# Kernel tuning notes

Hardware: AMD Instinct MI355X
Metric: run time of the kernel (lower is better)

## Reference

```python
import jax, jax.numpy as jnp
import numpy as np

H, W = 480, 640
ICP_W = 10.0
N_ITER = 20
FTOL = 1e-3
XTOL = 1e-8
DIST_THR = 200.0 / 15.0
NORMAL_THR = 0.94


def _skew(w):
    z = jnp.zeros((), w.dtype)
    return jnp.stack([
        jnp.stack([z, -w[2], w[1]]),
        jnp.stack([w[2], z, -w[0]]),
        jnp.stack([-w[1], w[0], z]),
    ])


def _exp_se3(xi):
    # xi = (v, w); SE3 exponential map (lie_se3_to_SE3)
    v, w = xi[:3], xi[3:]
    th2 = jnp.sum(w * w)
    th = jnp.sqrt(th2)
    small = th < 1e-8
    ths = jnp.where(small, 1.0, th)
    A = jnp.where(small, 1.0 - th2 / 6.0, jnp.sin(ths) / ths)
    B = jnp.where(small, 0.5 - th2 / 24.0, (1.0 - jnp.cos(ths)) / (ths * ths))
    C = jnp.where(small, 1.0 / 6.0 - th2 / 120.0, (ths - jnp.sin(ths)) / (ths * ths * ths))
    Wx = _skew(w)
    W2 = Wx @ Wx
    R = jnp.eye(3, dtype=xi.dtype) + A * Wx + B * W2
    V = jnp.eye(3, dtype=xi.dtype) + B * Wx + C * W2
    t = V @ v
    T = jnp.eye(4, dtype=xi.dtype)
    T = T.at[:3, :3].set(R).at[:3, 3].set(t)
    return T


def _bilinear(img, u, v):
    # img [H,W]; u,v [N] float pixel coords
    u0 = jnp.floor(u)
    v0 = jnp.floor(v)
    du = u - u0
    dv = v - v0
    u0i = jnp.clip(u0.astype(jnp.int32), 0, W - 1)
    u1i = jnp.clip(u0i + 1, 0, W - 1)
    v0i = jnp.clip(v0.astype(jnp.int32), 0, H - 1)
    v1i = jnp.clip(v0i + 1, 0, H - 1)
    I00 = img[v0i, u0i]; I01 = img[v0i, u1i]
    I10 = img[v1i, u0i]; I11 = img[v1i, u1i]
    return (I00 * (1 - du) + I01 * du) * (1 - dv) + (I10 * (1 - du) + I11 * du) * dv


def _forward(depth_ref, normals_ref, gray_ref, gray_target, points_target, normals_target, intrinsics):
    dt = depth_ref.dtype
    fx, fy = intrinsics[0, 0], intrinsics[1, 1]
    cx, cy = intrinsics[0, 2], intrinsics[1, 2]
    vv, uu = jnp.meshgrid(jnp.arange(H, dtype=dt), jnp.arange(W, dtype=dt), indexing='ij')
    Z = depth_ref
    # ref PointCloud.from_depth: backprojection [N,3]
    P = jnp.stack([(uu - cx) / fx * Z, (vv - cy) / fy * Z, Z], -1).reshape(-1, 3)
    Nr = normals_ref.reshape(-1, 3)
    Ir = gray_ref.reshape(-1)
    gy_img, gx_img = jnp.gradient(gray_target)  # d/dv, d/du
    Nflt = jnp.asarray(H * W, dt)

    def step(carry, _):
        x, conv, cost = carry
        T = _exp_se3(x)
        R, t = T[:3, :3], T[:3, 3]
        Pt = P @ R.T + t  # transformed ref points [N,3]
        Zt = Pt[:, 2]
        okz = Zt > 1e-6
        Zs = jnp.where(okz, Zt, 1.0)
        u = fx * Pt[:, 0] / Zs + cx
        v = fy * Pt[:, 1] / Zs + cy
        inb = okz & (u >= 0) & (u <= W - 1) & (v >= 0) & (v <= H - 1)
        ui = jnp.clip(jnp.round(u).astype(jnp.int32), 0, W - 1)
        vi = jnp.clip(jnp.round(v).astype(jnp.int32), 0, H - 1)
        # --- ICP point-to-plane, projective association ---
        q = points_target[vi, ui]    # [N,3]
        nq = normals_target[vi, ui]  # [N,3]
        d = Pt - q
        nref_rot = Nr @ R.T
        valid_icp = inb & (jnp.sum(d * d, -1) < DIST_THR ** 2) & (jnp.sum(nref_rot * nq, -1) > NORMAL_THR)
        m_icp = valid_icp.astype(dt)
        r_icp = jnp.sum(nq * d, -1) * m_icp                              # [N]
        J_icp = jnp.concatenate([nq, jnp.cross(Pt, nq)], -1) * m_icp[:, None]  # [N,6]
        # --- RGB photometric ---
        m_rgb = inb.astype(dt)
        It = _bilinear(gray_target, u, v)
        r_rgb = (It - Ir) * m_rgb
        gxs = _bilinear(gx_img, u, v)
        gys = _bilinear(gy_img, u, v)
        # grad_I * d(projection)/d(point)
        gp = jnp.stack([
            gxs * fx / Zs,
            gys * fy / Zs,
            -(gxs * fx * Pt[:, 0] + gys * fy * Pt[:, 1]) / (Zs * Zs),
        ], -1)
        J_rgb = jnp.concatenate([gp, jnp.cross(Pt, gp)], -1) * m_rgb[:, None]
        # --- normal equations ---
        A = ICP_W * (J_icp.T @ J_icp) + J_rgb.T @ J_rgb
        b = ICP_W * (J_icp.T @ r_icp) + J_rgb.T @ r_rgb
        x0 = jnp.linalg.solve(A + 1e-9 * jnp.eye(6, dtype=dt), b)
        new_cost = ICP_W * jnp.sum(r_icp ** 2) / Nflt + jnp.sum(r_rgb ** 2) / Nflt
        c = conv | (new_cost < FTOL) | (jnp.linalg.norm(x0) < XTOL * (XTOL + jnp.linalg.norm(x)))
        x_new = jnp.where(c, x, x - x0)
        cost_new = jnp.where(conv, cost, new_cost)
        return (x_new, c, cost_new), None

    init = (jnp.zeros(6, dt), jnp.array(False), jnp.asarray(0.0, dt))
    (x, conv, cost), _ = jax.lax.scan(step, init, None, length=N_ITER)
    return _exp_se3(x), cost


def setup_inputs() -> dict:
    key = jax.random.key(0)
    ks = jax.random.split(key, 6)
    intrinsics = jnp.array([[525.0, 0.0, 319.5], [0.0, 525.0, 239.5], [0.0, 0.0, 1.0]], jnp.float32)
    fx, fy, cx, cy = 525.0, 525.0, 319.5, 239.5
    depth_ref = 0.5 + 1.5 * jax.random.uniform(ks[0], (H, W), jnp.float32)
    depth_t = 0.5 + 1.5 * jax.random.uniform(ks[1], (H, W), jnp.float32)
    vv, uu = jnp.meshgrid(jnp.arange(H, dtype=jnp.float32), jnp.arange(W, dtype=jnp.float32), indexing='ij')
    points_target = jnp.stack([(uu - cx) / fx * depth_t, (vv - cy) / fy * depth_t, depth_t], -1)
    def mk_normals(k):
        n = 0.1 * jax.random.normal(k, (H, W, 3), jnp.float32) + jnp.array([0.0, 0.0, -1.0])
        return n / jnp.linalg.norm(n, axis=-1, keepdims=True)
    normals_ref = mk_normals(ks[2])
    normals_target = mk_normals(ks[3])
    gray_ref = jax.random.uniform(ks[4], (H, W), jnp.float32)
    gray_target = jax.random.uniform(ks[5], (H, W), jnp.float32)
    return {
        'depth_ref': depth_ref,
        'normals_ref': normals_ref,
        'gray_ref': gray_ref,
        'gray_target': gray_target,
        'points_target': points_target,
        'normals_target': normals_target,
        'intrinsics': intrinsics,
    }


def reference(depth_ref, normals_ref, gray_ref, gray_target, points_target, normals_target, intrinsics):
    return _forward(depth_ref, normals_ref, gray_ref, gray_target, points_target, normals_target, intrinsics)
```

## Files before the change

### kernel.cpp

```cpp
#include <hip/hip_runtime.h>
#include <math.h>

#define HH 480
#define WW 640
#define NPIX (HH*WW)
#define NACC 29
#define TPB_B 512
#define NB_B 600
#define TPB_C 256
#define PB 600
#define CH 75

#define WS_P 512
#define WS_G4 18432
#define WS_NR (WS_G4 + NPIX*4)
#define WS_PZ (WS_NR + NPIX*4)
#define WS_BIG_END (WS_PZ + NPIX*4)

__device__ __forceinline__ float gradu(const float* g, int v, int u) {
    const float* row = g + v * WW;
    if (u == 0)      return row[1] - row[0];
    if (u == WW - 1) return row[WW - 1] - row[WW - 2];
    return 0.5f * (row[u + 1] - row[u - 1]);
}
__device__ __forceinline__ float gradv(const float* g, int v, int u) {
    if (v == 0)      return g[WW + u] - g[u];
    if (v == HH - 1) return g[(HH - 1) * WW + u] - g[(HH - 2) * WW + u];
    return 0.5f * (g[(v + 1) * WW + u] - g[(v - 1) * WW + u]);
}

__device__ void exp_se3_f32(const float* xi, float* T) {
    float v0 = xi[0], v1 = xi[1], v2 = xi[2];
    float w0 = xi[3], w1 = xi[4], w2 = xi[5];
    float th2 = w0 * w0 + w1 * w1 + w2 * w2;
    float th = sqrtf(th2);
    bool small = th < 1e-8f;
    float ths = small ? 1.0f : th;
    float A = small ? (1.0f - th2 / 6.0f) : (sinf(ths) / ths);
    float B = small ? (0.5f - th2 / 24.0f) : ((1.0f - cosf(ths)) / (ths * ths));
    float C = small ? (1.0f / 6.0f - th2 / 120.0f) : ((ths - sinf(ths)) / (ths * ths * ths));
    float Wx[9] = { 0.f, -w2,  w1,
                    w2,  0.f, -w0,
                   -w1,  w0,  0.f };
    float W2[9];
    #pragma unroll
    for (int i = 0; i < 3; i++)
        #pragma unroll
        for (int j = 0; j < 3; j++) {
            float s = 0.f;
            #pragma unroll
            for (int k = 0; k < 3; k++) s += Wx[i * 3 + k] * Wx[k * 3 + j];
            W2[i * 3 + j] = s;
        }
    float R[9], V[9];
    #pragma unroll
    for (int i = 0; i < 9; i++) {
        float id = (i == 0 || i == 4 || i == 8) ? 1.0f : 0.0f;
        R[i] = id + A * Wx[i] + B * W2[i];
        V[i] = id + B * Wx[i] + C * W2[i];
    }
    float t0 = V[0] * v0 + V[1] * v1 + V[2] * v2;
    float t1 = V[3] * v0 + V[4] * v1 + V[5] * v2;
    float t2 = V[6] * v0 + V[7] * v1 + V[8] * v2;
    T[0] = R[0]; T[1] = R[1]; T[2]  = R[2]; T[3]  = t0;
    T[4] = R[3]; T[5] = R[4]; T[6]  = R[5]; T[7]  = t1;
    T[8] = R[6]; T[9] = R[7]; T[10] = R[8]; T[11] = t2;
    T[12] = 0.f; T[13] = 0.f; T[14] = 0.f; T[15] = 1.f;
}

__device__ __forceinline__ void accum_point(float* acc, const float* J, float r, float w, int costslot) {
    int k = 0;
    #pragma unroll
    for (int i = 0; i < 6; i++) {
        #pragma unroll
        for (int j = i; j < 6; j++) { acc[k] += w * (J[i] * J[j]); k++; }
        acc[21 + i] += w * (J[i] * r);
    }
    acc[costslot] += r * r;
}

template <int PACKED>
__global__ __launch_bounds__(TPB_B) void pack_init(
    const float* __restrict__ depth_ref,
    const float* __restrict__ normals_ref,
    const float* __restrict__ gray_target,
    const float* __restrict__ points_target,
    const float* __restrict__ normals_target,
    float* __restrict__ ws)
{
    if (blockIdx.x == 0 && threadIdx.x == 0) {
        ws[0] = 1.f; ws[1] = 0.f; ws[2] = 0.f;
        ws[3] = 0.f; ws[4] = 1.f; ws[5] = 0.f;
        ws[6] = 0.f; ws[7] = 0.f; ws[8] = 1.f;
        ws[9] = 0.f; ws[10] = 0.f; ws[11] = 0.f;
        ws[12] = 0.f; ws[13] = 0.f;
        #pragma unroll
        for (int i = 0; i < 6; i++) ws[16 + i] = 0.f;
    }
    if (PACKED) {
        int p = blockIdx.x * TPB_B + threadIdx.x;
        int v = p / WW, u = p - v * WW;
        float4* g4  = (float4*)(ws + WS_G4);
        float4* nr4 = (float4*)(ws + WS_NR);
        float4* pz4 = (float4*)(ws + WS_PZ);
        float4 c;
        c.x = gray_target[p];
        c.y = gradu(gray_target, v, u);
        c.z = gradv(gray_target, v, u);
        c.w = 0.f;
        g4[p] = c;
        float4 n;
        n.x = normals_ref[3 * p];
        n.y = normals_ref[3 * p + 1];
        n.z = normals_ref[3 * p + 2];
        n.w = depth_ref[p];
        nr4[p] = n;
        float4 z;
        z.x = points_target[3 * p + 2];
        z.y = normals_target[3 * p];
        z.z = normals_target[3 * p + 1];
        z.w = normals_target[3 * p + 2];
        pz4[p] = z;
    }
}

template <int PACKED>
__global__ __launch_bounds__(TPB_B) void map_reduce(
    const float* __restrict__ depth_ref,
    const float* __restrict__ normals_ref,
    const float* __restrict__ gray_ref,
    const float* __restrict__ gray_target,
    const float* __restrict__ points_target,
    const float* __restrict__ normals_target,
    const float* __restrict__ K,
    float* __restrict__ ws)
{
    const int tid = threadIdx.x;
    const int bid = blockIdx.x;
    const float fx = K[0], cx = K[2], fy = K[4], cy = K[5];
    const float4* g4  = (const float4*)(ws + WS_G4);
    const float4* nr4 = (const float4*)(ws + WS_NR);
    const float4* pz4 = (const float4*)(ws + WS_PZ);

    __shared__ float spose[12];
    __shared__ float lds[8][NACC];
    if (tid < 12) spose[tid] = ws[tid];
    __syncthreads();
    const float R00 = spose[0], R01 = spose[1], R02 = spose[2];
    const float R10 = spose[3], R11 = spose[4], R12 = spose[5];
    const float R20 = spose[6], R21 = spose[7], R22 = spose[8];
    const float t0 = spose[9], t1 = spose[10], t2 = spose[11];

    float acc[NACC];
    #pragma unroll
    for (int i = 0; i < NACC; i++) acc[i] = 0.f;

    {
        int p = bid * TPB_B + tid;
        int vv = p / WW;
        int uu = p - vv * WW;

        float nr0, nr1, nr2, Z;
        if (PACKED) {
            float4 n = nr4[p];
            nr0 = n.x; nr1 = n.y; nr2 = n.z; Z = n.w;
        } else {
            Z = depth_ref[p];
            nr0 = normals_ref[3 * p]; nr1 = normals_ref[3 * p + 1]; nr2 = normals_ref[3 * p + 2];
        }
        float Px = ((float)uu - cx) / fx * Z;
        float Py = ((float)vv - cy) / fy * Z;
        float Pz = Z;
        float Ptx = R00 * Px + R01 * Py + R02 * Pz + t0;
        float Pty = R10 * Px + R11 * Py + R12 * Pz + t1;
        float Ptz = R20 * Px + R21 * Py + R22 * Pz + t2;
        bool okz = Ptz > 1e-6f;
        float Zs = okz ? Ptz : 1.0f;
        float u = fx * Ptx / Zs + cx;
        float v = fy * Pty / Zs + cy;
        bool inb = okz && (u >= 0.f) && (u <= (float)(WW - 1)) && (v >= 0.f) && (v <= (float)(HH - 1));
        if (inb) {
            int ui = (int)rintf(u); ui = ui < 0 ? 0 : (ui > WW - 1 ? WW - 1 : ui);
            int vi = (int)rintf(v); vi = vi < 0 ? 0 : (vi > HH - 1 ? HH - 1 : vi);
            int ti = vi * WW + ui;
            float qx, qy, qz, nqx, nqy, nqz;
            if (PACKED) {
                float4 z = pz4[ti];
                qz = z.x; nqx = z.y; nqy = z.z; nqz = z.w;
                qx = (((float)ui) - cx) / fx * qz;
                qy = (((float)vi) - cy) / fy * qz;
            } else {
                qx = points_target[3 * ti]; qy = points_target[3 * ti + 1]; qz = points_target[3 * ti + 2];
                nqx = normals_target[3 * ti]; nqy = normals_target[3 * ti + 1]; nqz = normals_target[3 * ti + 2];
            }
            float dx = Ptx - qx, dy = Pty - qy, dz = Ptz - qz;
            float nrx = R00 * nr0 + R01 * nr1 + R02 * nr2;
            float nry = R10 * nr0 + R11 * nr1 + R12 * nr2;
            float nrz = R20 * nr0 + R21 * nr1 + R22 * nr2;
            const float DIST2 = (float)((200.0 / 15.0) * (200.0 / 15.0));
            if ((dx * dx + dy * dy + dz * dz) < DIST2 &&
                (nrx * nqx + nry * nqy + nrz * nqz) > 0.94f) {
                float r = nqx * dx + nqy * dy + nqz * dz;
                float J[6] = { nqx, nqy, nqz,
                               Pty * nqz - Ptz * nqy,
                               Ptz * nqx - Ptx * nqz,
                               Ptx * nqy - Pty * nqx };
                accum_point(acc, J, r, 10.0f, 27);
            }
            float u0f = floorf(u), v0f = floorf(v);
            float du = u - u0f, dv = v - v0f;
            int u0 = (int)u0f; u0 = u0 < 0 ? 0 : (u0 > WW - 1 ? WW - 1 : u0);
            int u1 = (u0 + 1 > WW - 1) ? WW - 1 : u0 + 1;
            int v0 = (int)v0f; v0 = v0 < 0 ? 0 : (v0 > HH - 1 ? HH - 1 : v0);
            int v1 = (v0 + 1 > HH - 1) ? HH - 1 : v0 + 1;
            int i00 = v0 * WW + u0, i01 = v0 * WW + u1, i10 = v1 * WW + u0, i11 = v1 * WW + u1;
            float I00, I01, I10, I11, gx00, gx01, gx10, gx11, gy00, gy01, gy10, gy11;
            if (PACKED) {
                float4 c00 = g4[i00], c01 = g4[i01], c10 = g4[i10], c11 = g4[i11];
                I00 = c00.x; gx00 = c00.y; gy00 = c00.z;
                I01 = c01.x; gx01 = c01.y; gy01 = c01.z;
                I10 = c10.x; gx10 = c10.y; gy10 = c10.z;
                I11 = c11.x; gx11 = c11.y; gy11 = c11.z;
            } else {
                const float* g = gray_target;
                I00 = g[i00]; I01 = g[i01]; I10 = g[i10]; I11 = g[i11];
                gx00 = gradu(g, v0, u0); gx01 = gradu(g, v0, u1);
                gx10 = gradu(g, v1, u0); gx11 = gradu(g, v1, u1);
                gy00 = gradv(g, v0, u0); gy01 = gradv(g, v0, u1);
                gy10 = gradv(g, v1, u0); gy11 = gradv(g, v1, u1);
            }
            float It  = (I00 * (1.f - du) + I01 * du) * (1.f - dv) + (I10 * (1.f - du) + I11 * du) * dv;
            float gxs = (gx00 * (1.f - du) + gx01 * du) * (1.f - dv) + (gx10 * (1.f - du) + gx11 * du) * dv;
            float gys = (gy00 * (1.f - du) + gy01 * du) * (1.f - dv) + (gy10 * (1.f - du) + gy11 * du) * dv;
            float rr = It - gray_ref[p];
            float gpx = gxs * fx / Zs;
            float gpy = gys * fy / Zs;
            float gpz = -(gxs * fx * Ptx + gys * fy * Pty) / (Zs * Zs);
            float J[6] = { gpx, gpy, gpz,
                           Pty * gpz - Ptz * gpy,
                           Ptz * gpx - Ptx * gpz,
                           Ptx * gpy - Pty * gpx };
            accum_point(acc, J, rr, 1.0f, 28);
        }
    }

    #pragma unroll
    for (int q = 0; q < NACC; q++) {
        float vq = acc[q];
        #pragma unroll
        for (int off = 32; off >= 1; off >>= 1) vq += __shfl_xor(vq, off);
        acc[q] = vq;
    }
    int wave = tid >> 6;
    int lane = tid & 63;
    if (lane == 0) {
        #pragma unroll
        for (int q = 0; q < NACC; q++) lds[wave][q] = acc[q];
    }
    __syncthreads();
    if (tid < NACC) {
        int q = tid;
        float s = ((lds[0][q] + lds[1][q]) + (lds[2][q] + lds[3][q]))
                + ((lds[4][q] + lds[5][q]) + (lds[6][q] + lds[7][q]));
        ws[WS_P + q * PB + bid] = s;
    }
}

__global__ __launch_bounds__(TPB_C) void solve_update(float* __restrict__ ws,
                                                      float* __restrict__ out,
                                                      int final_iter)
{
    __shared__ double part8[NACC * 8];
    __shared__ double sums[NACC];
    int tid = threadIdx.x;
    const float* part = ws + WS_P;
    if (tid < NACC * 8) {
        int q = tid >> 3, s = tid & 7;
        const float* row = part + q * PB + s * CH;
        double a0 = 0.0, a1 = 0.0, a2 = 0.0, a3 = 0.0;
        int i = 0;
        for (; i + 4 <= CH; i += 4) {
            a0 += (double)row[i];
            a1 += (double)row[i + 1];
            a2 += (double)row[i + 2];
            a3 += (double)row[i + 3];
        }
        for (; i < CH; i++) a0 += (double)row[i];
        part8[tid] = ((a0 + a1) + (a2 + a3));
    }
    __syncthreads();
    if (tid < NACC) {
        double sm = 0.0;
        #pragma unroll
        for (int s = 0; s < 8; s++) sm += part8[tid * 8 + s];
        sums[tid] = sm;
    }
    __syncthreads();
    if (tid == 0) {
        double M[6][7];
        int k = 0;
        for (int i = 0; i < 6; i++)
            for (int j = i; j < 6; j++) { M[i][j] = sums[k]; M[j][i] = sums[k]; k++; }
        for (int i = 0; i < 6; i++) { M[i][6] = sums[21 + i]; M[i][i] += 1e-9; }
        double new_cost = 10.0 * sums[27] / (double)NPIX + sums[28] / (double)NPIX;

        for (int c = 0; c < 6; c++) {
            int piv = c; double mx = fabs(M[c][c]);
            for (int r2 = c + 1; r2 < 6; r2++) {
                double a = fabs(M[r2][c]);
                if (a > mx) { mx = a; piv = r2; }
            }
            if (piv != c)
                for (int j2 = 0; j2 < 7; j2++) { double tmp = M[c][j2]; M[c][j2] = M[piv][j2]; M[piv][j2] = tmp; }
            double inv = 1.0 / M[c][c];
            for (int r2 = c + 1; r2 < 6; r2++) {
                double f = M[r2][c] * inv;
                for (int j2 = c; j2 < 7; j2++) M[r2][j2] -= f * M[c][j2];
            }
        }
        double x0[6];
        for (int i = 5; i >= 0; i--) {
            double s = M[i][6];
            for (int j = i + 1; j < 6; j++) s -= M[i][j] * x0[j];
            x0[i] = s / M[i][i];
        }

        double nx0 = 0.0, nx = 0.0;
        float xf[6];
        for (int i = 0; i < 6; i++) {
            xf[i] = ws[16 + i];
            nx0 += x0[i] * x0[i];
            nx  += (double)xf[i] * (double)xf[i];
        }
        nx0 = sqrt(nx0); nx = sqrt(nx);
        bool convold = (ws[12] != 0.f);
        bool c2 = convold || (new_cost < 1e-3) || (nx0 < 1e-8 * (1e-8 + nx));
        float xn[6];
        for (int i = 0; i < 6; i++)
            xn[i] = c2 ? xf[i] : (float)((double)xf[i] - x0[i]);
        for (int i = 0; i < 6; i++) ws[16 + i] = xn[i];
        ws[12] = c2 ? 1.f : 0.f;
        if (!convold) ws[13] = (float)new_cost;

        float T[16];
        exp_se3_f32(xn, T);
        ws[0] = T[0]; ws[1] = T[1]; ws[2]  = T[2];
        ws[3] = T[4]; ws[4] = T[5]; ws[5]  = T[6];
        ws[6] = T[8]; ws[7] = T[9]; ws[8]  = T[10];
        ws[9] = T[3]; ws[10] = T[7]; ws[11] = T[11];

        if (final_iter) {
            for (int i = 0; i < 16; i++) out[i] = T[i];
            out[16] = ws[13];
        }
    }
}

extern "C" void kernel_launch(void* const* d_in, const int* in_sizes, int n_in,
                              void* d_out, int out_size, void* d_ws, size_t ws_size,
                              hipStream_t stream) {
    const float* depth_ref      = (const float*)d_in[0];
    const float* normals_ref    = (const float*)d_in[1];
    const float* gray_ref       = (const float*)d_in[2];
    const float* gray_target    = (const float*)d_in[3];
    const float* points_target  = (const float*)d_in[4];
    const float* normals_target = (const float*)d_in[5];
    const float* K              = (const float*)d_in[6];
    float* ws  = (float*)d_ws;
    float* out = (float*)d_out;

    bool big = ws_size >= (size_t)WS_BIG_END * sizeof(float);
    if (big) {
        hipLaunchKernelGGL((pack_init<1>), dim3(NB_B), dim3(TPB_B), 0, stream,
                           depth_ref, normals_ref, gray_target,
                           points_target, normals_target, ws);
        for (int it = 0; it < 20; ++it) {
            hipLaunchKernelGGL((map_reduce<1>), dim3(NB_B), dim3(TPB_B), 0, stream,
                               depth_ref, normals_ref, gray_ref, gray_target,
                               points_target, normals_target, K, ws);
            hipLaunchKernelGGL(solve_update, dim3(1), dim3(TPB_C), 0, stream,
                               ws, out, (it == 19) ? 1 : 0);
        }
    } else {
        hipLaunchKernelGGL((pack_init<0>), dim3(NB_B), dim3(TPB_B), 0, stream,
                           depth_ref, normals_ref, gray_target,
                           points_target, normals_target, ws);
        for (int it = 0; it < 20; ++it) {
            hipLaunchKernelGGL((map_reduce<0>), dim3(NB_B), dim3(TPB_B), 0, stream,
                               depth_ref, normals_ref, gray_ref, gray_target,
                               points_target, normals_target, K, ws);
            hipLaunchKernelGGL(solve_update, dim3(1), dim3(TPB_C), 0, stream,
                               ws, out, (it == 19) ? 1 : 0);
        }
    }
}
```

Before: 444.5 us.

## Fuse per-iteration solve into map kernel via last-block reduction

Removes the separate single-block solve_update launch after each map_reduce pass. Each block now stores its partial sums with agent-scope atomic stores and bumps a per-iteration counter, and the last block to finish does the double-precision final reduction, the 6x6 solve and the pose update. This cuts 20 small kernel launches and the dependency gaps between them. The final reduction is split 16 ways instead of 8, and launch bounds now ask for 4 blocks per CU. It relies on relaxed atomics with no explicit release/acquire fence, which is a subtle memory-ordering risk.

Result: slower. 595.0 us (+33.9%).

```diff
diff --git a/kernel.cpp b/kernel.cpp
--- a/kernel.cpp
+++ b/kernel.cpp
@@ -7,15 +7,22 @@
 #define NACC 29
 #define TPB_B 512
 #define NB_B 600
-#define TPB_C 256
 #define PB 600
-#define CH 75
+#define NSPL 16
+#define CHS 38
 
 #define WS_P 512
 #define WS_G4 18432
 #define WS_NR (WS_G4 + NPIX*4)
 #define WS_PZ (WS_NR + NPIX*4)
 #define WS_BIG_END (WS_PZ + NPIX*4)
+
+__device__ __forceinline__ float ld_f_sc1(const float* p) {
+    return __hip_atomic_load(p, __ATOMIC_RELAXED, __HIP_MEMORY_SCOPE_AGENT);
+}
+__device__ __forceinline__ void st_f_sc1(float* p, float v) {
+    __hip_atomic_store(p, v, __ATOMIC_RELAXED, __HIP_MEMORY_SCOPE_AGENT);
+}
 
 __device__ __forceinline__ float gradu(const float* g, int v, int u) {
     const float* row = g + v * WW;
@@ -125,7 +132,7 @@
 }
 
 template <int PACKED>
-__global__ __launch_bounds__(TPB_B) void map_reduce(
+__global__ __launch_bounds__(TPB_B, 4) void map_fused(
     const float* __restrict__ depth_ref,
     const float* __restrict__ normals_ref,
     const float* __restrict__ gray_ref,
@@ -133,7 +140,9 @@
     const float* __restrict__ points_target,
     const float* __restrict__ normals_target,
     const float* __restrict__ K,
-    float* __restrict__ ws)
+    float* __restrict__ ws,
+    float* __restrict__ out,
+    int it)
 {
     const int tid = threadIdx.x;
     const int bid = blockIdx.x;
@@ -141,9 +150,12 @@
     const float4* g4  = (const float4*)(ws + WS_G4);
     const float4* nr4 = (const float4*)(ws + WS_NR);
     const float4* pz4 = (const float4*)(ws + WS_PZ);
+    float* pbuf = ws + WS_P;
+    int* cnt = (int*)ws + 32 + it;
 
     __shared__ float spose[12];
     __shared__ float lds[8][NACC];
+    __shared__ int slast;
     if (tid < 12) spose[tid] = ws[tid];
     __syncthreads();
     const float R00 = spose[0], R01 = spose[1], R02 = spose[2];
@@ -262,42 +274,46 @@
         int q = tid;
         float s = ((lds[0][q] + lds[1][q]) + (lds[2][q] + lds[3][q]))
                 + ((lds[4][q] + lds[5][q]) + (lds[6][q] + lds[7][q]));
-        ws[WS_P + q * PB + bid] = s;
-    }
-}
-
-__global__ __launch_bounds__(TPB_C) void solve_update(float* __restrict__ ws,
-                                                      float* __restrict__ out,
-                                                      int final_iter)
-{
-    __shared__ double part8[NACC * 8];
+        st_f_sc1(&pbuf[q * PB + bid], s);
+    }
+    __syncthreads();
+    if (tid == 0) {
+        int a = __hip_atomic_fetch_add(cnt, 1, __ATOMIC_RELAXED, __HIP_MEMORY_SCOPE_AGENT);
+        slast = (a == NB_B - 1) ? 1 : 0;
+    }
+    __syncthreads();
+    if (!slast) return;
+
+    __shared__ double p16[NACC * NSPL];
     __shared__ double sums[NACC];
-    int tid = threadIdx.x;
-    const float* part = ws + WS_P;
-    if (tid < NACC * 8) {
-        int q = tid >> 3, s = tid & 7;
-        const float* row = part + q * PB + s * CH;
+    __shared__ double M[6][7];
+    __shared__ double x0s[6];
+    if (tid < NACC * NSPL) {
+        int q = tid >> 4, s = tid & 15;
+        int lo = s * CHS;
+        int hi = lo + CHS; if (hi > PB) hi = PB;
+        const float* row = pbuf + q * PB + lo;
         double a0 = 0.0, a1 = 0.0, a2 = 0.0, a3 = 0.0;
+        int n = hi - lo;
         int i = 0;
-        for (; i + 4 <= CH; i += 4) {
-            a0 += (double)row[i];
-            a1 += (double)row[i + 1];
-            a2 += (double)row[i + 2];
-            a3 += (double)row[i + 3];
-        }
-        for (; i < CH; i++) a0 += (double)row[i];
-        part8[tid] = ((a0 + a1) + (a2 + a3));
+        for (; i + 4 <= n; i += 4) {
+            a0 += (double)ld_f_sc1(&row[i]);
+            a1 += (double)ld_f_sc1(&row[i + 1]);
+            a2 += (double)ld_f_sc1(&row[i + 2]);
+            a3 += (double)ld_f_sc1(&row[i + 3]);
+        }
+        for (; i < n; i++) a0 += (double)ld_f_sc1(&row[i]);
+        p16[tid] = ((a0 + a1) + (a2 + a3));
     }
     __syncthreads();
     if (tid < NACC) {
         double sm = 0.0;
         #pragma unroll
-        for (int s = 0; s < 8; s++) sm += part8[tid * 8 + s];
+        for (int s = 0; s < NSPL; s++) sm += p16[tid * NSPL + s];
         sums[tid] = sm;
     }
     __syncthreads();
     if (tid == 0) {
-        double M[6][7];
         int k = 0;
         for (int i = 0; i < 6; i++)
             for (int j = i; j < 6; j++) { M[i][j] = sums[k]; M[j][i] = sums[k]; k++; }
@@ -318,18 +334,17 @@
                 for (int j2 = c; j2 < 7; j2++) M[r2][j2] -= f * M[c][j2];
             }
         }
-        double x0[6];
         for (int i = 5; i >= 0; i--) {
             double s = M[i][6];
-            for (int j = i + 1; j < 6; j++) s -= M[i][j] * x0[j];
-            x0[i] = s / M[i][i];
+            for (int j = i + 1; j < 6; j++) s -= M[i][j] * x0s[j];
+            x0s[i] = s / M[i][i];
         }
 
         double nx0 = 0.0, nx = 0.0;
         float xf[6];
         for (int i = 0; i < 6; i++) {
             xf[i] = ws[16 + i];
-            nx0 += x0[i] * x0[i];
+            nx0 += x0s[i] * x0s[i];
             nx  += (double)xf[i] * (double)xf[i];
         }
         nx0 = sqrt(nx0); nx = sqrt(nx);
@@ -337,7 +352,7 @@
         bool c2 = convold || (new_cost < 1e-3) || (nx0 < 1e-8 * (1e-8 + nx));
         float xn[6];
         for (int i = 0; i < 6; i++)
-            xn[i] = c2 ? xf[i] : (float)((double)xf[i] - x0[i]);
+            xn[i] = c2 ? xf[i] : (float)((double)xf[i] - x0s[i]);
         for (int i = 0; i < 6; i++) ws[16 + i] = xn[i];
         ws[12] = c2 ? 1.f : 0.f;
         if (!convold) ws[13] = (float)new_cost;
@@ -349,7 +364,7 @@
         ws[6] = T[8]; ws[7] = T[9]; ws[8]  = T[10];
         ws[9] = T[3]; ws[10] = T[7]; ws[11] = T[11];
 
-        if (final_iter) {
+        if (it == 19) {
             for (int i = 0; i < 16; i++) out[i] = T[i];
             out[16] = ws[13];
         }
@@ -369,28 +384,26 @@
     float* ws  = (float*)d_ws;
     float* out = (float*)d_out;
 
+    hipMemsetAsync(d_ws, 0, 256, stream);
+
     bool big = ws_size >= (size_t)WS_BIG_END * sizeof(float);
     if (big) {
         hipLaunchKernelGGL((pack_init<1>), dim3(NB_B), dim3(TPB_B), 0, stream,
                            depth_ref, normals_ref, gray_target,
                            points_target, normals_target, ws);
         for (int it = 0; it < 20; ++it) {
-            hipLaunchKernelGGL((map_reduce<1>), dim3(NB_B), dim3(TPB_B), 0, stream,
+            hipLaunchKernelGGL((map_fused<1>), dim3(NB_B), dim3(TPB_B), 0, stream,
                                depth_ref, normals_ref, gray_ref, gray_target,
-                               points_target, normals_target, K, ws);
-            hipLaunchKernelGGL(solve_update, dim3(1), dim3(TPB_C), 0, stream,
-                               ws, out, (it == 19) ? 1 : 0);
+                               points_target, normals_target, K, ws, out, it);
         }
     } else {
         hipLaunchKernelGGL((pack_init<0>), dim3(NB_B), dim3(TPB_B), 0, stream,
                            depth_ref, normals_ref, gray_target,
                            points_target, normals_target, ws);
         for (int it = 0; it < 20; ++it) {
-            hipLaunchKernelGGL((map_reduce<0>), dim3(NB_B), dim3(TPB_B), 0, stream,
+            hipLaunchKernelGGL((map_fused<0>), dim3(NB_B), dim3(TPB_B), 0, stream,
                                depth_ref, normals_ref, gray_ref, gray_target,
-                               points_target, normals_target, K, ws);
-            hipLaunchKernelGGL(solve_update, dim3(1), dim3(TPB_C), 0, stream,
-                               ws, out, (it == 19) ? 1 : 0);
-        }
-    }
-}
+                               points_target, normals_target, K, ws, out, it);
+        }
+    }
+}
```
